# Performance work log

Hardware: AMD Instinct MI355X
Metric: run time of the kernel (lower is better)

The kernel has to match this reference:

```python
import jax, jax.numpy as jnp
import numpy as np

B, S, H, E = 4, 4096, 2048, 16
ED = H // 4
LN_EPS = 1e-5
ROUTING_SCALE = 0.01
NEG_INF = -1e9


def setup_inputs() -> dict:
    key = jax.random.key(0)
    ks = jax.random.split(key, 10)
    std = 0.02
    w_std = 1.0 / np.sqrt(H)  # roughly nn.Linear default scale
    return {
        "hidden_states": jax.random.normal(ks[0], (B, S, H), jnp.float32),
        "layer_embeddings": jax.random.normal(ks[1], (E, H), jnp.float32) * std,
        "centrality_embeddings": jax.random.normal(ks[2], (E, H), jnp.float32) * std,
        "spatial_embeddings": jax.random.normal(ks[3], (E + 1, 1), jnp.float32) * std,
        "edge_embeddings": jax.random.normal(ks[4], (E, ED), jnp.float32) * std,
        "ln_gamma": jnp.ones((H,), jnp.float32),
        "ln_beta": jnp.zeros((H,), jnp.float32),
        "Wq": jax.random.normal(ks[5], (H, H), jnp.float32) * w_std,
        "bq": jnp.zeros((H,), jnp.float32),
        "Wk": jax.random.normal(ks[6], (H, H), jnp.float32) * w_std,
        "bk": jnp.zeros((H,), jnp.float32),
        "Wv": jax.random.normal(ks[7], (H, H), jnp.float32) * w_std,
        "bv": jnp.zeros((H,), jnp.float32),
        "current_layer": 0,  # current_depth == 0 path: used_experts = {0}
        "available_mask": jnp.ones((E,), jnp.int32).at[0].set(0),
    }


def _layer_norm(x, g, b):
    mu = jnp.mean(x, axis=-1, keepdims=True)
    var = jnp.mean(jnp.square(x - mu), axis=-1, keepdims=True)
    return (x - mu) * jax.lax.rsqrt(var + LN_EPS) * g + b


def reference(hidden_states, layer_embeddings, centrality_embeddings,
              spatial_embeddings, edge_embeddings, ln_gamma, ln_beta,
              Wq, bq, Wk, bk, Wv, bv, current_layer, available_mask):
    avail = available_mask.astype(jnp.float32)  # [E]

    # --- attention scores over experts ---
    current_embed = layer_embeddings[current_layer]                 # [H]
    normed = _layer_norm(hidden_states, ln_gamma, ln_beta)          # [B,S,H]
    hidden_mean = jnp.mean(normed, axis=1)                          # [B,H]
    query_input = current_embed + hidden_mean                       # [B,H]
    layer_features = layer_embeddings + centrality_embeddings       # [E,H]

    q = query_input @ Wq.T + bq                                     # [B,H]
    k = layer_features @ Wk.T + bk                                  # [E,H]
    # v is computed in the original but never used downstream of scores
    _v = layer_features @ Wv.T + bv                                 # [E,H]

    attention = (q @ k.T) / np.sqrt(H)                              # [B,E]

    # --- spatial bias ---
    idx = jnp.arange(E)
    distances = jnp.abs(idx - current_layer)                        # [E]
    spatial_bias = spatial_embeddings[distances, 0]                 # [E]

    # --- edge bias: vectorized form of the per-expert loop ---
    # sum over i in available, i != current: (edge_emb[i] @ edge_emb.T) / max(dist_i,1)
    ew = edge_embeddings @ edge_embeddings.T                        # [E,E]
    scale = 1.0 / jnp.maximum(distances, 1).astype(jnp.float32)     # [E]
    row_mask = avail * (idx != current_layer).astype(jnp.float32)   # [E]
    edge_bias = jnp.einsum("i,ij->j", row_mask * scale, ew)         # [E]

    scores = attention + spatial_bias + edge_bias                   # [B,E]
    scores = jnp.where(avail > 0, scores, NEG_INF)                  # mask unavailable

    # --- routing loss (KL to uniform-over-available, batchmean) ---
    probs = jax.nn.softmax(scores, axis=-1)                         # [B,E]
    num_avail = jnp.sum(avail)
    t = 1.0 / num_avail                                             # scalar target prob
    probs_safe = jnp.clip(probs, 1e-10)
    kl = jnp.sum(t * (jnp.log(t) - jnp.log(probs_safe))) / B
    routing_loss = kl * ROUTING_SCALE

    next_idx = jnp.argmax(probs[0], axis=-1)
    return routing_loss, probs, next_idx
```

## Files before the change

### kernel.cpp

```cpp
#include <hip/hip_runtime.h>
#include <hip/hip_bf16.h>

#define DEV __device__ __forceinline__

constexpr float INV_SQRT_H = 0.022097086912079608f;

constexpr size_t WS_PART = 0;
constexpr size_t WS_MU   = WS_PART + (size_t)512 * 2048;
constexpr size_t WS_QI   = WS_MU + 2048;
constexpr size_t WS_Q    = WS_QI + 4 * 2048;
constexpr size_t WS_K    = WS_Q + 4 * 2048;
constexpr size_t WS_LF   = WS_K + 16 * 2048;
constexpr size_t WS_ATT  = WS_LF + 16 * 2048 / 2;

DEV bool is_bf16_probe(const void* g) {
    return ((const unsigned int*)g)[0] == 0x3F803F80u;
}

template <bool BF16>
DEV void load8(const void* base, size_t idx, float* o) {
    if constexpr (BF16) {
        const unsigned short* p = (const unsigned short*)base + idx;
        uint4 u = *(const uint4*)p;
        o[0] = __uint_as_float(u.x << 16); o[1] = __uint_as_float(u.x & 0xFFFF0000u);
        o[2] = __uint_as_float(u.y << 16); o[3] = __uint_as_float(u.y & 0xFFFF0000u);
        o[4] = __uint_as_float(u.z << 16); o[5] = __uint_as_float(u.z & 0xFFFF0000u);
        o[6] = __uint_as_float(u.w << 16); o[7] = __uint_as_float(u.w & 0xFFFF0000u);
    } else {
        const float* p = (const float*)base + idx;
        float4 a = *(const float4*)p;
        float4 b = *(const float4*)(p + 4);
        o[0] = a.x; o[1] = a.y; o[2] = a.z; o[3] = a.w;
        o[4] = b.x; o[5] = b.y; o[6] = b.z; o[7] = b.w;
    }
}

template <bool BF16>
DEV float ld1(const void* base, size_t idx) {
    if constexpr (BF16) {
        unsigned int v = ((const unsigned short*)base)[idx];
        return __uint_as_float(v << 16);
    } else {
        return ((const float*)base)[idx];
    }
}

template <bool BF16>
DEV void st1(void* base, size_t idx, float v) {
    if constexpr (BF16) {
        ((__hip_bfloat16*)base)[idx] = __float2bfloat16(v);
    } else {
        ((float*)base)[idx] = v;
    }
}

template <bool BF16>
DEV void k1_body(const void* hidden, float* ws) {
    int bid = blockIdx.x;
    int b = bid >> 7;
    int chunk = bid & 127;
    int wave = threadIdx.x >> 6, lane = threadIdx.x & 63;

    float acc[32];
#pragma unroll
    for (int i = 0; i < 32; ++i) acc[i] = 0.f;
    float accmu = 0.f;

    for (int r = 0; r < 8; ++r) {
        int s = chunk * 32 + wave * 8 + r;
        size_t base = ((size_t)(b * 4096 + s)) * 2048;
        float x[32];
#pragma unroll
        for (int j = 0; j < 4; ++j)
            load8<BF16>(hidden, base + j * 512 + lane * 8, &x[j * 8]);
        float s1 = 0.f, s2 = 0.f;
#pragma unroll
        for (int i = 0; i < 32; ++i) { s1 += x[i]; s2 += x[i] * x[i]; }
#pragma unroll
        for (int off = 1; off < 64; off <<= 1) {
            s1 += __shfl_xor(s1, off);
            s2 += __shfl_xor(s2, off);
        }
        float mu = s1 * (1.f / 2048.f);
        float var = s2 * (1.f / 2048.f) - mu * mu;
        float rsig = rsqrtf(var + 1e-5f);
        accmu += rsig * mu;
#pragma unroll
        for (int i = 0; i < 32; ++i) acc[i] += rsig * x[i];
    }

    __shared__ float lds[4 * 2048];
#pragma unroll
    for (int j = 0; j < 4; ++j) {
        float4 v0 = make_float4(acc[j * 8 + 0], acc[j * 8 + 1], acc[j * 8 + 2], acc[j * 8 + 3]);
        float4 v1 = make_float4(acc[j * 8 + 4], acc[j * 8 + 5], acc[j * 8 + 6], acc[j * 8 + 7]);
        *(float4*)&lds[wave * 2048 + j * 512 + lane * 8 + 0] = v0;
        *(float4*)&lds[wave * 2048 + j * 512 + lane * 8 + 4] = v1;
    }
    __syncthreads();
    int c0 = threadIdx.x * 8;
    float4 s0, s1v;
    s0.x = lds[0 * 2048 + c0 + 0] + lds[1 * 2048 + c0 + 0] + lds[2 * 2048 + c0 + 0] + lds[3 * 2048 + c0 + 0];
    s0.y = lds[0 * 2048 + c0 + 1] + lds[1 * 2048 + c0 + 1] + lds[2 * 2048 + c0 + 1] + lds[3 * 2048 + c0 + 1];
    s0.z = lds[0 * 2048 + c0 + 2] + lds[1 * 2048 + c0 + 2] + lds[2 * 2048 + c0 + 2] + lds[3 * 2048 + c0 + 2];
    s0.w = lds[0 * 2048 + c0 + 3] + lds[1 * 2048 + c0 + 3] + lds[2 * 2048 + c0 + 3] + lds[3 * 2048 + c0 + 3];
    s1v.x = lds[0 * 2048 + c0 + 4] + lds[1 * 2048 + c0 + 4] + lds[2 * 2048 + c0 + 4] + lds[3 * 2048 + c0 + 4];
    s1v.y = lds[0 * 2048 + c0 + 5] + lds[1 * 2048 + c0 + 5] + lds[2 * 2048 + c0 + 5] + lds[3 * 2048 + c0 + 5];
    s1v.z = lds[0 * 2048 + c0 + 6] + lds[1 * 2048 + c0 + 6] + lds[2 * 2048 + c0 + 6] + lds[3 * 2048 + c0 + 6];
    s1v.w = lds[0 * 2048 + c0 + 7] + lds[1 * 2048 + c0 + 7] + lds[2 * 2048 + c0 + 7] + lds[3 * 2048 + c0 + 7];
    float* part = ws + WS_PART + (size_t)bid * 2048 + c0;
    *(float4*)(part + 0) = s0;
    *(float4*)(part + 4) = s1v;
    if (lane == 0) ws[WS_MU + bid * 4 + wave] = accmu;
}

__global__ __launch_bounds__(256) void k1(const void* hidden, const void* probe, float* ws) {
    if (is_bf16_probe(probe)) k1_body<true>(hidden, ws);
    else k1_body<false>(hidden, ws);
}

template <bool BF16>
DEV void k1b_body(float* ws, const void* gamma, const void* beta, const void* lemb,
                  const void* cemb, const int* curp) {
    int bid = blockIdx.x, tid = threadIdx.x;
    if (bid < 64) {
        int b = bid >> 4, cc = bid & 15;
        __shared__ float smu[4];
        __shared__ float comb[128];
        float m = ws[WS_MU + b * 512 + tid] + ws[WS_MU + b * 512 + 256 + tid];
#pragma unroll
        for (int off = 1; off < 64; off <<= 1) m += __shfl_xor(m, off);
        if ((tid & 63) == 0) smu[tid >> 6] = m;
        int col = cc * 128 + (tid & 127);
        int p0 = (tid < 128) ? 0 : 64;
        float a = 0.f;
#pragma unroll 4
        for (int p = p0; p < p0 + 64; ++p)
            a += ws[WS_PART + ((size_t)(b * 128 + p)) * 2048 + col];
        if (tid >= 128) comb[tid - 128] = a;
        __syncthreads();
        if (tid < 128) {
            float accmu = smu[0] + smu[1] + smu[2] + smu[3];
            float tot = a + comb[tid];
            float hm = ld1<BF16>(gamma, col) * (tot - accmu) * (1.f / 4096.f) +
                       ld1<BF16>(beta, col);
            int cur = curp[0];
            ws[WS_QI + b * 2048 + col] = ld1<BF16>(lemb, (size_t)cur * 2048 + col) + hm;
        }
    } else {
        int e = bid - 64, c0 = tid * 8;
        __hip_bfloat16* lf = (__hip_bfloat16*)(ws + WS_LF);
#pragma unroll
        for (int q = 0; q < 8; ++q) {
            int c = c0 + q;
            float v = ld1<BF16>(lemb, (size_t)e * 2048 + c) + ld1<BF16>(cemb, (size_t)e * 2048 + c);
            lf[e * 2048 + c] = __float2bfloat16(v);
        }
    }
}

__global__ __launch_bounds__(256) void k1b(float* ws, const void* gamma, const void* beta,
                                           const void* lemb, const void* cemb, const int* curp) {
    if (is_bf16_probe(gamma)) k1b_body<true>(ws, gamma, beta, lemb, cemb, curp);
    else k1b_body<false>(ws, gamma, beta, lemb, cemb, curp);
}

template <bool BF16>
DEV void k2_body(float* ws, const void* Wq, const void* Wk, const void* bq, const void* bk) {
    int bid = blockIdx.x;
    int wave = threadIdx.x >> 6, lane = threadIdx.x & 63;
    if (bid < 512) {
        int h = bid * 4 + wave;
        float acc[4];
#pragma unroll
        for (int b = 0; b < 4; ++b) acc[b] = 0.f;
#pragma unroll
        for (int ci = 0; ci < 4; ++ci) {
            int c0 = ci * 512 + lane * 8;
            float w8[8];
            load8<BF16>(Wq, (size_t)h * 2048 + c0, w8);
#pragma unroll
            for (int b = 0; b < 4; ++b) {
                const float* qi = ws + WS_QI + (size_t)b * 2048 + c0;
                float4 u1 = *(const float4*)qi;
                float4 u2 = *(const float4*)(qi + 4);
                acc[b] += w8[0] * u1.x + w8[1] * u1.y + w8[2] * u1.z + w8[3] * u1.w +
                          w8[4] * u2.x + w8[5] * u2.y + w8[6] * u2.z + w8[7] * u2.w;
            }
        }
#pragma unroll
        for (int b = 0; b < 4; ++b)
#pragma unroll
            for (int off = 1; off < 64; off <<= 1) acc[b] += __shfl_xor(acc[b], off);
        if (lane == 0) {
            float bias = ld1<BF16>(bq, h);
#pragma unroll
            for (int b = 0; b < 4; ++b) ws[WS_Q + (size_t)b * 2048 + h] = acc[b] + bias;
        }
    } else {
        int h = (bid - 512) * 4 + wave;
        const void* lf = (const void*)(ws + WS_LF);
        float acc[16];
#pragma unroll
        for (int e = 0; e < 16; ++e) acc[e] = 0.f;
#pragma unroll
        for (int ci = 0; ci < 4; ++ci) {
            int c0 = ci * 512 + lane * 8;
            float w8[8];
            load8<BF16>(Wk, (size_t)h * 2048 + c0, w8);
#pragma unroll
            for (int e = 0; e < 16; ++e) {
                float l8[8];
                load8<true>(lf, (size_t)e * 2048 + c0, l8);
                acc[e] += w8[0] * l8[0] + w8[1] * l8[1] + w8[2] * l8[2] + w8[3] * l8[3] +
                          w8[4] * l8[4] + w8[5] * l8[5] + w8[6] * l8[6] + w8[7] * l8[7];
            }
        }
#pragma unroll
        for (int e = 0; e < 16; ++e)
#pragma unroll
            for (int off = 1; off < 64; off <<= 1) acc[e] += __shfl_xor(acc[e], off);
        if (lane == 0) {
            float bias = ld1<BF16>(bk, h);
#pragma unroll
            for (int e = 0; e < 16; ++e) ws[WS_K + (size_t)e * 2048 + h] = acc[e] + bias;
        }
    }
}

__global__ __launch_bounds__(256) void k2(float* ws, const void* Wq, const void* Wk,
                                          const void* bq, const void* bk, const void* probe) {
    if (is_bf16_probe(probe)) k2_body<true>(ws, Wq, Wk, bq, bk);
    else k2_body<false>(ws, Wq, Wk, bq, bk);
}

template <bool BF16>
DEV void k3_body(float* ws, const void* spat, const void* edge, const int* curp,
                 const int* availp, void* out) {
    __shared__ float att[64];
    int wave = threadIdx.x >> 6, lane64 = threadIdx.x & 63;
    int b = wave;

    float q[32];
#pragma unroll
    for (int ci = 0; ci < 4; ++ci) {
        const float* qp = ws + WS_Q + (size_t)b * 2048 + ci * 512 + lane64 * 8;
        float4 a = *(const float4*)qp;
        float4 c = *(const float4*)(qp + 4);
        q[ci * 8 + 0] = a.x; q[ci * 8 + 1] = a.y; q[ci * 8 + 2] = a.z; q[ci * 8 + 3] = a.w;
        q[ci * 8 + 4] = c.x; q[ci * 8 + 5] = c.y; q[ci * 8 + 6] = c.z; q[ci * 8 + 7] = c.w;
    }
    for (int e = 0; e < 16; ++e) {
        float acc = 0.f;
#pragma unroll
        for (int ci = 0; ci < 4; ++ci) {
            const float* kp = ws + WS_K + (size_t)e * 2048 + ci * 512 + lane64 * 8;
            float4 x1 = *(const float4*)kp;
            float4 x2 = *(const float4*)(kp + 4);
            acc += q[ci * 8 + 0] * x1.x + q[ci * 8 + 1] * x1.y +
                   q[ci * 8 + 2] * x1.z + q[ci * 8 + 3] * x1.w +
                   q[ci * 8 + 4] * x2.x + q[ci * 8 + 5] * x2.y +
                   q[ci * 8 + 6] * x2.z + q[ci * 8 + 7] * x2.w;
        }
#pragma unroll
        for (int off = 1; off < 64; off <<= 1) acc += __shfl_xor(acc, off);
        if (lane64 == 0) att[b * 16 + e] = acc * INV_SQRT_H;
    }
    __syncthreads();
    if (wave != 0) return;

    int lane = lane64;
    int cur = curp[0];
    int av[16];
    int navail = 0;
#pragma unroll
    for (int i = 0; i < 16; ++i) { av[i] = availp[i]; navail += (av[i] != 0); }

    int d0 = lane * 8;
    float w8[8];
#pragma unroll
    for (int qq = 0; qq < 8; ++qq) w8[qq] = 0.f;
    for (int i = 0; i < 16; ++i) {
        if (av[i] && i != cur) {
            int dist = i > cur ? i - cur : cur - i;
            float coef = 1.f / (float)(dist > 1 ? dist : 1);
            float e8[8];
            load8<BF16>(edge, (size_t)i * 512 + d0, e8);
#pragma unroll
            for (int qq = 0; qq < 8; ++qq) w8[qq] += coef * e8[qq];
        }
    }
    float bias[16];
    for (int j = 0; j < 16; ++j) {
        float e8[8];
        load8<BF16>(edge, (size_t)j * 512 + d0, e8);
        float p = w8[0] * e8[0] + w8[1] * e8[1] + w8[2] * e8[2] + w8[3] * e8[3] +
                  w8[4] * e8[4] + w8[5] * e8[5] + w8[6] * e8[6] + w8[7] * e8[7];
#pragma unroll
        for (int off = 1; off < 64; off <<= 1) p += __shfl_xor(p, off);
        bias[j] = p;
    }

    int e = lane & 15;
    int dist_e = e > cur ? e - cur : cur - e;
    float sp = ld1<BF16>(spat, dist_e);
    float s = att[lane] + sp + bias[e];
    if (!av[e]) s = -1e9f;

    float m = s;
#pragma unroll
    for (int off = 1; off < 16; off <<= 1) m = fmaxf(m, __shfl_xor(m, off));
    float ex = expf(s - m);
    float sum = ex;
#pragma unroll
    for (int off = 1; off < 16; off <<= 1) sum += __shfl_xor(sum, off);
    float p = ex / sum;
    st1<BF16>(out, 1 + lane, p);

    float t = 1.f / (float)navail;
    float term = t * (logf(t) - logf(fmaxf(p, 1e-10f)));
    float tot = term;
#pragma unroll
    for (int off = 1; off < 64; off <<= 1) tot += __shfl_xor(tot, off);
    if (lane == 0) st1<BF16>(out, 0, tot * (0.01f / 4.f));

    float m2 = p;
#pragma unroll
    for (int off = 1; off < 16; off <<= 1) m2 = fmaxf(m2, __shfl_xor(m2, off));
    int cand = (p == m2 && lane < 16) ? e : 1000;
#pragma unroll
    for (int off = 1; off < 16; off <<= 1) cand = min(cand, __shfl_xor(cand, off));
    if (lane == 0) st1<BF16>(out, 65, (float)cand);
}

__global__ __launch_bounds__(256) void k3(float* ws, const void* spat, const void* edge,
                                          const void* probe, const int* curp,
                                          const int* availp, void* out) {
    if (is_bf16_probe(probe)) k3_body<true>(ws, spat, edge, curp, availp, out);
    else k3_body<false>(ws, spat, edge, curp, availp, out);
}

extern "C" void kernel_launch(void* const* d_in, const int* in_sizes, int n_in,
                              void* d_out, int out_size, void* d_ws, size_t ws_size,
                              hipStream_t stream) {
    const void* hidden = d_in[0];
    const void* lemb   = d_in[1];
    const void* cemb   = d_in[2];
    const void* spat   = d_in[3];
    const void* edge   = d_in[4];
    const void* gamma  = d_in[5];
    const void* beta   = d_in[6];
    const void* Wq     = d_in[7];
    const void* bq     = d_in[8];
    const void* Wk     = d_in[9];
    const void* bk     = d_in[10];
    const int* curp    = (const int*)d_in[13];
    const int* availp  = (const int*)d_in[14];
    float* ws = (float*)d_ws;

    k1<<<512, 256, 0, stream>>>(hidden, gamma, ws);
    k1b<<<80, 256, 0, stream>>>(ws, gamma, beta, lemb, cemb, curp);
    k2<<<1024, 256, 0, stream>>>(ws, Wq, Wk, bq, bk, gamma);
    k3<<<1, 256, 0, stream>>>(ws, spat, edge, gamma, curp, availp, d_out);
}
```

Before: 292.1 us.

## Co-schedule K projection with layernorm stats and double stats-kernel parallelism

Moves the independent K-projection (Wk times layer+centrality embeddings) into the same launch as the hidden-state layernorm reduction, so the Wk read overlaps the large hidden-state stream instead of running after it. It also doubles the reduction grid to 1024 blocks with 16 rows each, and computes layer_features inline rather than materialising a bf16 copy. The price is a larger partial-sum buffer that the follow-up reduce kernel must read, twice as many rows per column. The Q projection becomes its own launch after the reduce, so the kernel count stays the same.

```diff
diff --git a/kernel.cpp b/kernel.cpp
--- a/kernel.cpp
+++ b/kernel.cpp
@@ -6,12 +6,10 @@
 constexpr float INV_SQRT_H = 0.022097086912079608f;
 
 constexpr size_t WS_PART = 0;
-constexpr size_t WS_MU   = WS_PART + (size_t)512 * 2048;
-constexpr size_t WS_QI   = WS_MU + 2048;
+constexpr size_t WS_MU   = WS_PART + (size_t)1024 * 2048;
+constexpr size_t WS_QI   = WS_MU + 4096;
 constexpr size_t WS_Q    = WS_QI + 4 * 2048;
 constexpr size_t WS_K    = WS_Q + 4 * 2048;
-constexpr size_t WS_LF   = WS_K + 16 * 2048;
-constexpr size_t WS_ATT  = WS_LF + 16 * 2048 / 2;
 
 DEV bool is_bf16_probe(const void* g) {
     return ((const unsigned int*)g)[0] == 0x3F803F80u;
@@ -55,151 +53,68 @@
 }
 
 template <bool BF16>
-DEV void k1_body(const void* hidden, float* ws) {
-    int bid = blockIdx.x;
-    int b = bid >> 7;
-    int chunk = bid & 127;
-    int wave = threadIdx.x >> 6, lane = threadIdx.x & 63;
-
-    float acc[32];
-#pragma unroll
-    for (int i = 0; i < 32; ++i) acc[i] = 0.f;
-    float accmu = 0.f;
-
-    for (int r = 0; r < 8; ++r) {
-        int s = chunk * 32 + wave * 8 + r;
-        size_t base = ((size_t)(b * 4096 + s)) * 2048;
-        float x[32];
-#pragma unroll
-        for (int j = 0; j < 4; ++j)
-            load8<BF16>(hidden, base + j * 512 + lane * 8, &x[j * 8]);
-        float s1 = 0.f, s2 = 0.f;
-#pragma unroll
-        for (int i = 0; i < 32; ++i) { s1 += x[i]; s2 += x[i] * x[i]; }
-#pragma unroll
-        for (int off = 1; off < 64; off <<= 1) {
-            s1 += __shfl_xor(s1, off);
-            s2 += __shfl_xor(s2, off);
-        }
-        float mu = s1 * (1.f / 2048.f);
-        float var = s2 * (1.f / 2048.f) - mu * mu;
-        float rsig = rsqrtf(var + 1e-5f);
-        accmu += rsig * mu;
-#pragma unroll
-        for (int i = 0; i < 32; ++i) acc[i] += rsig * x[i];
-    }
-
-    __shared__ float lds[4 * 2048];
-#pragma unroll
-    for (int j = 0; j < 4; ++j) {
-        float4 v0 = make_float4(acc[j * 8 + 0], acc[j * 8 + 1], acc[j * 8 + 2], acc[j * 8 + 3]);
-        float4 v1 = make_float4(acc[j * 8 + 4], acc[j * 8 + 5], acc[j * 8 + 6], acc[j * 8 + 7]);
-        *(float4*)&lds[wave * 2048 + j * 512 + lane * 8 + 0] = v0;
-        *(float4*)&lds[wave * 2048 + j * 512 + lane * 8 + 4] = v1;
-    }
-    __syncthreads();
-    int c0 = threadIdx.x * 8;
-    float4 s0, s1v;
-    s0.x = lds[0 * 2048 + c0 + 0] + lds[1 * 2048 + c0 + 0] + lds[2 * 2048 + c0 + 0] + lds[3 * 2048 + c0 + 0];
-    s0.y = lds[0 * 2048 + c0 + 1] + lds[1 * 2048 + c0 + 1] + lds[2 * 2048 + c0 + 1] + lds[3 * 2048 + c0 + 1];
-    s0.z = lds[0 * 2048 + c0 + 2] + lds[1 * 2048 + c0 + 2] + lds[2 * 2048 + c0 + 2] + lds[3 * 2048 + c0 + 2];
-    s0.w = lds[0 * 2048 + c0 + 3] + lds[1 * 2048 + c0 + 3] + lds[2 * 2048 + c0 + 3] + lds[3 * 2048 + c0 + 3];
-    s1v.x = lds[0 * 2048 + c0 + 4] + lds[1 * 2048 + c0 + 4] + lds[2 * 2048 + c0 + 4] + lds[3 * 2048 + c0 + 4];
-    s1v.y = lds[0 * 2048 + c0 + 5] + lds[1 * 2048 + c0 + 5] + lds[2 * 2048 + c0 + 5] + lds[3 * 2048 + c0 + 5];
-    s1v.z = lds[0 * 2048 + c0 + 6] + lds[1 * 2048 + c0 + 6] + lds[2 * 2048 + c0 + 6] + lds[3 * 2048 + c0 + 6];
-    s1v.w = lds[0 * 2048 + c0 + 7] + lds[1 * 2048 + c0 + 7] + lds[2 * 2048 + c0 + 7] + lds[3 * 2048 + c0 + 7];
-    float* part = ws + WS_PART + (size_t)bid * 2048 + c0;
-    *(float4*)(part + 0) = s0;
-    *(float4*)(part + 4) = s1v;
-    if (lane == 0) ws[WS_MU + bid * 4 + wave] = accmu;
-}
-
-__global__ __launch_bounds__(256) void k1(const void* hidden, const void* probe, float* ws) {
-    if (is_bf16_probe(probe)) k1_body<true>(hidden, ws);
-    else k1_body<false>(hidden, ws);
-}
-
-template <bool BF16>
-DEV void k1b_body(float* ws, const void* gamma, const void* beta, const void* lemb,
-                  const void* cemb, const int* curp) {
-    int bid = blockIdx.x, tid = threadIdx.x;
-    if (bid < 64) {
-        int b = bid >> 4, cc = bid & 15;
-        __shared__ float smu[4];
-        __shared__ float comb[128];
-        float m = ws[WS_MU + b * 512 + tid] + ws[WS_MU + b * 512 + 256 + tid];
-#pragma unroll
-        for (int off = 1; off < 64; off <<= 1) m += __shfl_xor(m, off);
-        if ((tid & 63) == 0) smu[tid >> 6] = m;
-        int col = cc * 128 + (tid & 127);
-        int p0 = (tid < 128) ? 0 : 64;
-        float a = 0.f;
-#pragma unroll 4
-        for (int p = p0; p < p0 + 64; ++p)
-            a += ws[WS_PART + ((size_t)(b * 128 + p)) * 2048 + col];
-        if (tid >= 128) comb[tid - 128] = a;
-        __syncthreads();
-        if (tid < 128) {
-            float accmu = smu[0] + smu[1] + smu[2] + smu[3];
-            float tot = a + comb[tid];
-            float hm = ld1<BF16>(gamma, col) * (tot - accmu) * (1.f / 4096.f) +
-                       ld1<BF16>(beta, col);
-            int cur = curp[0];
-            ws[WS_QI + b * 2048 + col] = ld1<BF16>(lemb, (size_t)cur * 2048 + col) + hm;
-        }
-    } else {
-        int e = bid - 64, c0 = tid * 8;
-        __hip_bfloat16* lf = (__hip_bfloat16*)(ws + WS_LF);
-#pragma unroll
-        for (int q = 0; q < 8; ++q) {
-            int c = c0 + q;
-            float v = ld1<BF16>(lemb, (size_t)e * 2048 + c) + ld1<BF16>(cemb, (size_t)e * 2048 + c);
-            lf[e * 2048 + c] = __float2bfloat16(v);
-        }
-    }
-}
-
-__global__ __launch_bounds__(256) void k1b(float* ws, const void* gamma, const void* beta,
-                                           const void* lemb, const void* cemb, const int* curp) {
-    if (is_bf16_probe(gamma)) k1b_body<true>(ws, gamma, beta, lemb, cemb, curp);
-    else k1b_body<false>(ws, gamma, beta, lemb, cemb, curp);
-}
-
-template <bool BF16>
-DEV void k2_body(float* ws, const void* Wq, const void* Wk, const void* bq, const void* bk) {
+DEV void kA_body(const void* hidden, const void* lemb, const void* cemb,
+                 const void* Wk, const void* bk, float* ws) {
     int bid = blockIdx.x;
     int wave = threadIdx.x >> 6, lane = threadIdx.x & 63;
-    if (bid < 512) {
-        int h = bid * 4 + wave;
-        float acc[4];
-#pragma unroll
-        for (int b = 0; b < 4; ++b) acc[b] = 0.f;
-#pragma unroll
-        for (int ci = 0; ci < 4; ++ci) {
-            int c0 = ci * 512 + lane * 8;
-            float w8[8];
-            load8<BF16>(Wq, (size_t)h * 2048 + c0, w8);
-#pragma unroll
-            for (int b = 0; b < 4; ++b) {
-                const float* qi = ws + WS_QI + (size_t)b * 2048 + c0;
-                float4 u1 = *(const float4*)qi;
-                float4 u2 = *(const float4*)(qi + 4);
-                acc[b] += w8[0] * u1.x + w8[1] * u1.y + w8[2] * u1.z + w8[3] * u1.w +
-                          w8[4] * u2.x + w8[5] * u2.y + w8[6] * u2.z + w8[7] * u2.w;
+
+    if (bid < 1024) {
+        int b = bid >> 8;
+        int chunk = bid & 255;
+
+        float acc[32];
+#pragma unroll
+        for (int i = 0; i < 32; ++i) acc[i] = 0.f;
+        float accmu = 0.f;
+
+        for (int r = 0; r < 4; ++r) {
+            int s = chunk * 16 + wave * 4 + r;
+            size_t base = ((size_t)(b * 4096 + s)) * 2048;
+            float x[32];
+#pragma unroll
+            for (int j = 0; j < 4; ++j)
+                load8<BF16>(hidden, base + j * 512 + lane * 8, &x[j * 8]);
+            float s1 = 0.f, s2 = 0.f;
+#pragma unroll
+            for (int i = 0; i < 32; ++i) { s1 += x[i]; s2 += x[i] * x[i]; }
+#pragma unroll
+            for (int off = 1; off < 64; off <<= 1) {
+                s1 += __shfl_xor(s1, off);
+                s2 += __shfl_xor(s2, off);
             }
-        }
-#pragma unroll
-        for (int b = 0; b < 4; ++b)
-#pragma unroll
-            for (int off = 1; off < 64; off <<= 1) acc[b] += __shfl_xor(acc[b], off);
-        if (lane == 0) {
-            float bias = ld1<BF16>(bq, h);
-#pragma unroll
-            for (int b = 0; b < 4; ++b) ws[WS_Q + (size_t)b * 2048 + h] = acc[b] + bias;
-        }
+            float mu = s1 * (1.f / 2048.f);
+            float var = s2 * (1.f / 2048.f) - mu * mu;
+            float rsig = rsqrtf(var + 1e-5f);
+            accmu += rsig * mu;
+#pragma unroll
+            for (int i = 0; i < 32; ++i) acc[i] += rsig * x[i];
+        }
+
+        __shared__ float lds[4 * 2048];
+#pragma unroll
+        for (int j = 0; j < 4; ++j) {
+            float4 v0 = make_float4(acc[j * 8 + 0], acc[j * 8 + 1], acc[j * 8 + 2], acc[j * 8 + 3]);
+            float4 v1 = make_float4(acc[j * 8 + 4], acc[j * 8 + 5], acc[j * 8 + 6], acc[j * 8 + 7]);
+            *(float4*)&lds[wave * 2048 + j * 512 + lane * 8 + 0] = v0;
+            *(float4*)&lds[wave * 2048 + j * 512 + lane * 8 + 4] = v1;
+        }
+        __syncthreads();
+        int c0 = threadIdx.x * 8;
+        float4 s0, s1v;
+        s0.x = lds[0 * 2048 + c0 + 0] + lds[1 * 2048 + c0 + 0] + lds[2 * 2048 + c0 + 0] + lds[3 * 2048 + c0 + 0];
+        s0.y = lds[0 * 2048 + c0 + 1] + lds[1 * 2048 + c0 + 1] + lds[2 * 2048 + c0 + 1] + lds[3 * 2048 + c0 + 1];
+        s0.z = lds[0 * 2048 + c0 + 2] + lds[1 * 2048 + c0 + 2] + lds[2 * 2048 + c0 + 2] + lds[3 * 2048 + c0 + 2];
+        s0.w = lds[0 * 2048 + c0 + 3] + lds[1 * 2048 + c0 + 3] + lds[2 * 2048 + c0 + 3] + lds[3 * 2048 + c0 + 3];
+        s1v.x = lds[0 * 2048 + c0 + 4] + lds[1 * 2048 + c0 + 4] + lds[2 * 2048 + c0 + 4] + lds[3 * 2048 + c0 + 4];
+        s1v.y = lds[0 * 2048 + c0 + 5] + lds[1 * 2048 + c0 + 5] + lds[2 * 2048 + c0 + 5] + lds[3 * 2048 + c0 + 5];
+        s1v.z = lds[0 * 2048 + c0 + 6] + lds[1 * 2048 + c0 + 6] + lds[2 * 2048 + c0 + 6] + lds[3 * 2048 + c0 + 6];
+        s1v.w = lds[0 * 2048 + c0 + 7] + lds[1 * 2048 + c0 + 7] + lds[2 * 2048 + c0 + 7] + lds[3 * 2048 + c0 + 7];
+        float* part = ws + WS_PART + (size_t)bid * 2048 + c0;
+        *(float4*)(part + 0) = s0;
+        *(float4*)(part + 4) = s1v;
+        if (lane == 0) ws[WS_MU + bid * 4 + wave] = accmu;
     } else {
-        int h = (bid - 512) * 4 + wave;
-        const void* lf = (const void*)(ws + WS_LF);
+        int h = (bid - 1024) * 4 + wave;
         float acc[16];
 #pragma unroll
         for (int e = 0; e < 16; ++e) acc[e] = 0.f;
@@ -210,10 +125,11 @@
             load8<BF16>(Wk, (size_t)h * 2048 + c0, w8);
 #pragma unroll
             for (int e = 0; e < 16; ++e) {
-                float l8[8];
-                load8<true>(lf, (size_t)e * 2048 + c0, l8);
-                acc[e] += w8[0] * l8[0] + w8[1] * l8[1] + w8[2] * l8[2] + w8[3] * l8[3] +
-                          w8[4] * l8[4] + w8[5] * l8[5] + w8[6] * l8[6] + w8[7] * l8[7];
+                float l8[8], c8[8];
+                load8<BF16>(lemb, (size_t)e * 2048 + c0, l8);
+                load8<BF16>(cemb, (size_t)e * 2048 + c0, c8);
+#pragma unroll
+                for (int j = 0; j < 8; ++j) acc[e] += w8[j] * (l8[j] + c8[j]);
             }
         }
 #pragma unroll
@@ -228,14 +144,90 @@
     }
 }
 
-__global__ __launch_bounds__(256) void k2(float* ws, const void* Wq, const void* Wk,
-                                          const void* bq, const void* bk, const void* probe) {
-    if (is_bf16_probe(probe)) k2_body<true>(ws, Wq, Wk, bq, bk);
-    else k2_body<false>(ws, Wq, Wk, bq, bk);
-}
-
-template <bool BF16>
-DEV void k3_body(float* ws, const void* spat, const void* edge, const int* curp,
+__global__ __launch_bounds__(256) void kA(const void* hidden, const void* lemb,
+                                          const void* cemb, const void* Wk,
+                                          const void* bk, const void* probe, float* ws) {
+    if (is_bf16_probe(probe)) kA_body<true>(hidden, lemb, cemb, Wk, bk, ws);
+    else kA_body<false>(hidden, lemb, cemb, Wk, bk, ws);
+}
+
+template <bool BF16>
+DEV void kB_body(float* ws, const void* gamma, const void* beta, const void* lemb,
+                 const int* curp) {
+    int bid = blockIdx.x, tid = threadIdx.x;
+    int b = bid >> 4, cc = bid & 15;
+    __shared__ float smu[4];
+    __shared__ float comb[128];
+    float m = ws[WS_MU + b * 1024 + tid] + ws[WS_MU + b * 1024 + 256 + tid] +
+              ws[WS_MU + b * 1024 + 512 + tid] + ws[WS_MU + b * 1024 + 768 + tid];
+#pragma unroll
+    for (int off = 1; off < 64; off <<= 1) m += __shfl_xor(m, off);
+    if ((tid & 63) == 0) smu[tid >> 6] = m;
+    int col = cc * 128 + (tid & 127);
+    int p0 = (tid < 128) ? 0 : 128;
+    float a = 0.f;
+#pragma unroll 4
+    for (int p = p0; p < p0 + 128; ++p)
+        a += ws[WS_PART + ((size_t)(b * 256 + p)) * 2048 + col];
+    if (tid >= 128) comb[tid - 128] = a;
+    __syncthreads();
+    if (tid < 128) {
+        float accmu = smu[0] + smu[1] + smu[2] + smu[3];
+        float tot = a + comb[tid];
+        float hm = ld1<BF16>(gamma, col) * (tot - accmu) * (1.f / 4096.f) +
+                   ld1<BF16>(beta, col);
+        int cur = curp[0];
+        ws[WS_QI + b * 2048 + col] = ld1<BF16>(lemb, (size_t)cur * 2048 + col) + hm;
+    }
+}
+
+__global__ __launch_bounds__(256) void kB(float* ws, const void* gamma, const void* beta,
+                                          const void* lemb, const int* curp) {
+    if (is_bf16_probe(gamma)) kB_body<true>(ws, gamma, beta, lemb, curp);
+    else kB_body<false>(ws, gamma, beta, lemb, curp);
+}
+
+template <bool BF16>
+DEV void kC_body(float* ws, const void* Wq, const void* bq) {
+    int bid = blockIdx.x;
+    int wave = threadIdx.x >> 6, lane = threadIdx.x & 63;
+    int h = bid * 4 + wave;
+    float acc[4];
+#pragma unroll
+    for (int b = 0; b < 4; ++b) acc[b] = 0.f;
+#pragma unroll
+    for (int ci = 0; ci < 4; ++ci) {
+        int c0 = ci * 512 + lane * 8;
+        float w8[8];
+        load8<BF16>(Wq, (size_t)h * 2048 + c0, w8);
+#pragma unroll
+        for (int b = 0; b < 4; ++b) {
+            const float* qi = ws + WS_QI + (size_t)b * 2048 + c0;
+            float4 u1 = *(const float4*)qi;
+            float4 u2 = *(const float4*)(qi + 4);
+            acc[b] += w8[0] * u1.x + w8[1] * u1.y + w8[2] * u1.z + w8[3] * u1.w +
+                      w8[4] * u2.x + w8[5] * u2.y + w8[6] * u2.z + w8[7] * u2.w;
+        }
+    }
+#pragma unroll
+    for (int b = 0; b < 4; ++b)
+#pragma unroll
+        for (int off = 1; off < 64; off <<= 1) acc[b] += __shfl_xor(acc[b], off);
+    if (lane == 0) {
+        float bias = ld1<BF16>(bq, h);
+#pragma unroll
+        for (int b = 0; b < 4; ++b) ws[WS_Q + (size_t)b * 2048 + h] = acc[b] + bias;
+    }
+}
+
+__global__ __launch_bounds__(256) void kC(float* ws, const void* Wq, const void* bq,
+                                          const void* probe) {
+    if (is_bf16_probe(probe)) kC_body<true>(ws, Wq, bq);
+    else kC_body<false>(ws, Wq, bq);
+}
+
+template <bool BF16>
+DEV void kD_body(float* ws, const void* spat, const void* edge, const int* curp,
                  const int* availp, void* out) {
     __shared__ float att[64];
     int wave = threadIdx.x >> 6, lane64 = threadIdx.x & 63;
@@ -333,11 +325,11 @@
     if (lane == 0) st1<BF16>(out, 65, (float)cand);
 }
 
-__global__ __launch_bounds__(256) void k3(float* ws, const void* spat, const void* edge,
+__global__ __launch_bounds__(256) void kD(float* ws, const void* spat, const void* edge,
                                           const void* probe, const int* curp,
                                           const int* availp, void* out) {
-    if (is_bf16_probe(probe)) k3_body<true>(ws, spat, edge, curp, availp, out);
-    else k3_body<false>(ws, spat, edge, curp, availp, out);
+    if (is_bf16_probe(probe)) kD_body<true>(ws, spat, edge, curp, availp, out);
+    else kD_body<false>(ws, spat, edge, curp, availp, out);
 }
 
 extern "C" void kernel_launch(void* const* d_in, const int* in_sizes, int n_in,
@@ -358,8 +350,8 @@
     const int* availp  = (const int*)d_in[14];
     float* ws = (float*)d_ws;
 
-    k1<<<512, 256, 0, stream>>>(hidden, gamma, ws);
-    k1b<<<80, 256, 0, stream>>>(ws, gamma, beta, lemb, cemb, curp);
-    k2<<<1024, 256, 0, stream>>>(ws, Wq, Wk, bq, bk, gamma);
-    k3<<<1, 256, 0, stream>>>(ws, spat, edge, gamma, curp, availp, d_out);
-}
+    kA<<<1536, 256, 0, stream>>>(hidden, lemb, cemb, Wk, bk, gamma, ws);
+    kB<<<64, 256, 0, stream>>>(ws, gamma, beta, lemb, curp);
+    kC<<<512, 256, 0, stream>>>(ws, Wq, bq, gamma);
+    kD<<<1, 256, 0, stream>>>(ws, spat, edge, gamma, curp, availp, d_out);
+}
```

After: 297.6 us. No clear change (+1.9%).
